# Kernel tuning notes

Measured on AMD Instinct MI355X. Metric: run time of the kernel, lower is better.

The kernel has to match this reference:

```python
import jax, jax.numpy as jnp
import numpy as np

H = 32  # hidden size

def setup_inputs() -> dict:
    key = jax.random.key(0)
    ks = jax.random.split(key, 12)
    B, T = 64, 16384
    s = 0.1
    return {
        "x": jax.random.normal(ks[0], (B, T, 1), dtype=jnp.float32),
        "h_state": jax.random.normal(ks[1], (2, B, H), dtype=jnp.float32),
        "W_ih0": jax.random.normal(ks[2], (H, 1), dtype=jnp.float32) * s,
        "W_hh0": jax.random.normal(ks[3], (H, H), dtype=jnp.float32) * s,
        "b_ih0": jax.random.normal(ks[4], (H,), dtype=jnp.float32) * s,
        "b_hh0": jax.random.normal(ks[5], (H,), dtype=jnp.float32) * s,
        "W_ih1": jax.random.normal(ks[6], (H, H), dtype=jnp.float32) * s,
        "W_hh1": jax.random.normal(ks[7], (H, H), dtype=jnp.float32) * s,
        "b_ih1": jax.random.normal(ks[8], (H,), dtype=jnp.float32) * s,
        "b_hh1": jax.random.normal(ks[9], (H,), dtype=jnp.float32) * s,
        "W_out": jax.random.normal(ks[10], (1, H), dtype=jnp.float32) * s,
        "b_out": jax.random.normal(ks[11], (1,), dtype=jnp.float32) * s,
    }

def reference(x, h_state, W_ih0, W_hh0, b_ih0, b_hh0, W_ih1, W_hh1, b_ih1, b_hh1, W_out, b_out):
    # x: [B,T,1], h_state: [2,B,H]. PyTorch RNN (tanh):
    #   h_t = tanh(W_ih x_t + b_ih + W_hh h_{t-1} + b_hh)
    # Precompute the input projection for layer 0 outside the scan (memory-bound part).
    pre0 = jnp.einsum('bti,hi->tbh', x, W_ih0) + (b_ih0 + b_hh0)  # [T,B,H]
    b1 = b_ih1 + b_hh1

    def step(carry, p0):
        h0, h1 = carry
        h0n = jnp.tanh(p0 + h0 @ W_hh0.T)
        h1n = jnp.tanh(h0n @ W_ih1.T + b1 + h1 @ W_hh1.T)
        return (h0n, h1n), h1n

    (hf0, hf1), ys = jax.lax.scan(step, (h_state[0], h_state[1]), pre0)
    r_out = jnp.transpose(ys, (1, 0, 2)).reshape(-1, H)  # [B*T, H] (batch_first view)
    outs = r_out @ W_out.T + b_out                        # [B*T, 1]
    h_final = jnp.stack([hf0, hf1])                       # [2,B,H]
    return outs, h_final
```

## Files before the change

### kernel.cpp

```cpp
#include <hip/hip_runtime.h>


#define T_LEN 16384
#define B_SZ  64
#define NW    (T_LEN / 32)
#define TSC   2.885390082f

#if __has_builtin(__builtin_amdgcn_exp2f)
#define EXP2(x) __builtin_amdgcn_exp2f(x)
#else
#define EXP2(x) exp2f(x)
#endif

typedef _Float16 h2 __attribute__((ext_vector_type(2)));

__device__ __forceinline__ float rl(float v, int lane) {
  return __int_as_float(__builtin_amdgcn_readlane(__float_as_int(v), lane));
}

__device__ __forceinline__ h2 bperm_h2(int byteaddr, h2 v) {
  int o = __builtin_amdgcn_ds_bpermute(byteaddr, __builtin_bit_cast(int, v));
  return __builtin_bit_cast(h2, o);
}

__device__ __forceinline__ float pair_swap(float v) {
  int t = __builtin_amdgcn_update_dpp(0, __float_as_int(v), 0xB1, 0xF, 0xF, true);
  return __int_as_float(t);
}

__device__ __forceinline__ float tanh_pre(float v) {
  float e = EXP2(v);
  return fmaf(-2.f, __builtin_amdgcn_rcpf(e + 1.f), 1.f);
}

#if __has_builtin(__builtin_amdgcn_fdot2)
#define FDOT2(a, b, c) __builtin_amdgcn_fdot2((a), (b), (c), false)
#else
#define FDOT2(a, b, c) \
  fmaf((float)(a).x, (float)(b).x, fmaf((float)(a).y, (float)(b).y, (c)))
#endif

__device__ __forceinline__ h2 pack_state(float hcur) {
  float hsw = pair_swap(hcur);
#if __has_builtin(__builtin_amdgcn_cvt_pkrtz)
  return __builtin_bit_cast(h2, __builtin_amdgcn_cvt_pkrtz(hcur, hsw));
#else
  h2 p; p.x = (_Float16)hcur; p.y = (_Float16)hsw; return p;
#endif
}

#define BCASTB(dst, src_pk)                                  \
  _Pragma("unroll")                                          \
  for (int j_ = 0; j_ < 16; ++j_) (dst)[j_] = bperm_h2(8 * j_, (src_pk));

__device__ __forceinline__ float dot32h(const h2* w, const h2* hb, float seed) {
  float a0 = seed, a1 = 0.f, a2 = 0.f, a3 = 0.f;
#pragma unroll
  for (int j = 0; j < 4; ++j) {
    a0 = FDOT2(w[4 * j + 0], hb[4 * j + 0], a0);
    a1 = FDOT2(w[4 * j + 1], hb[4 * j + 1], a1);
    a2 = FDOT2(w[4 * j + 2], hb[4 * j + 2], a2);
    a3 = FDOT2(w[4 * j + 3], hb[4 * j + 3], a3);
  }
  return (a0 + a1) + (a2 + a3);
}

__global__ __launch_bounds__(128, 1) void rnn2_kernel(
    const float* __restrict__ x,    const float* __restrict__ hs,
    const float* __restrict__ Wih0, const float* __restrict__ Whh0,
    const float* __restrict__ bih0, const float* __restrict__ bhh0,
    const float* __restrict__ Wih1, const float* __restrict__ Whh1,
    const float* __restrict__ bih1, const float* __restrict__ bhh1,
    const float* __restrict__ Wout, const float* __restrict__ bout,
    float* __restrict__ out)
{
  __shared__ __align__(16) float uwin[2][1024];
  __shared__ __align__(16) float scratch[1024];

  const int  tid = (int)threadIdx.x;
  const int  wv  = tid >> 6;
  const int  m   = tid & 63;
  const int  r   = m & 31;
  const bool hi  = (m >= 32);
  const int  b   = (int)blockIdx.x;

  const float* pw = (wv == 0) ? (hi ? (Wih1 + r * 32) : (Whh0 + r * 32))
                              : (hi ? Wout : (Whh1 + r * 32));
  const float wsc = (wv == 0) ? TSC : (hi ? 1.f : TSC);
  h2 w[16];
#pragma unroll
  for (int k = 0; k < 8; ++k) {
    float4 q = ((const float4*)pw)[k];
    w[2 * k].x     = (_Float16)(q.x * wsc);
    w[2 * k].y     = (_Float16)(q.y * wsc);
    w[2 * k + 1].x = (_Float16)(q.z * wsc);
    w[2 * k + 1].y = (_Float16)(q.w * wsc);
  }

  float xw = 0.f, binv = 0.f;
  if (wv == 0) {
    if (hi) binv = TSC * (bih1[r] + bhh1[r]);
    else  { binv = TSC * (bih0[r] + bhh0[r]); xw = TSC * Wih0[r]; }
  }
  const float bo = bout[0];

  float hcur = (wv == 0) ? hs[b * 32 + r] : hs[2048 + b * 32 + r];

  float* up0 = hi ? &uwin[0][r] : &scratch[r];
  float* up1 = hi ? &uwin[1][r] : &scratch[r];

  const float* xb   = x + (size_t)b * T_LEN;
  float*       outp = out + (size_t)b * T_LEN;
  float*       hf   = out + (size_t)B_SZ * T_LEN;

  float obuf = 0.f;
  float xcur = 0.f;
  if (wv == 0) xcur = xb[m];

  for (int wdx = 0; wdx <= NW; ++wdx) {
    if (wv == 0) {
      if (wdx < NW) {
        float xnext = 0.f;
        if (wdx + 1 < NW) {
          int xi = 32 * (wdx + 1) + m; if (xi > T_LEN - 1) xi = T_LEN - 1;
          xnext = xb[xi];
        }
        float* up = (wdx & 1) ? up1 : up0;
#pragma unroll 8
        for (int t2 = 0; t2 < 32; ++t2) {
          h2 hpk = pack_state(hcur);
          h2 hb[16];
          BCASTB(hb, hpk);
          float xv   = rl(xcur, t2);
          float seed = fmaf(xv, xw, binv);
          float acc  = dot32h(w, hb, seed);
          up[t2 * 32] = acc;
          hcur = tanh_pre(acc);
        }
        xcur = xnext;
      }
    } else {
      if (wdx >= 1) {
        const int wb = wdx - 1;
        const float* ub = &uwin[wb & 1][r];
        float uval = ub[0];
#pragma unroll 8
        for (int t2 = 0; t2 < 32; ++t2) {
          const int t = 32 * wb - 1 + t2;
          h2 hpk = pack_state(hcur);
          h2 hb[16];
          BCASTB(hb, hpk);
          float sB  = hi ? 0.f : uval;
          float acc = dot32h(w, hb, sB);
          float unext = ub[((t2 + 1) & 31) * 32];
          float h1n = tanh_pre(acc);
          obuf = (m == 32 + t2) ? acc : obuf;
          if (t >= 0) hcur = h1n;
          uval = unext;
        }
        const int idx = 32 * wb - 2 + r;
        if (hi && idx >= 0) outp[idx] = obuf + bo;
      }
    }
    __syncthreads();
  }

  if (wv == 0) {
    h2 hpk = pack_state(hcur);
    h2 hb[16];
    BCASTB(hb, hpk);
    float acc = dot32h(w, hb, binv);
    if (hi) uwin[0][r] = acc;
    else    hf[b * 32 + r] = hcur;
  }
  __syncthreads();

  if (wv == 1) {
    float uT = uwin[0][r];
    h2 hpk = pack_state(hcur);
    h2 hb[16];
    BCASTB(hb, hpk);
    float acc = dot32h(w, hb, hi ? 0.f : uT);
    if (m == 32) outp[T_LEN - 2] = acc + bo;
    float h1T = tanh_pre(acc);
    h2 hpk2 = pack_state(h1T);
    h2 hb2[16];
    BCASTB(hb2, hpk2);
    float acc2 = dot32h(w, hb2, 0.f);
    if (m == 32) outp[T_LEN - 1] = acc2 + bo;
    if (!hi) hf[2048 + b * 32 + r] = h1T;
  }
}

extern "C" void kernel_launch(void* const* d_in, const int* in_sizes, int n_in,
                              void* d_out, int out_size, void* d_ws, size_t ws_size,
                              hipStream_t stream) {
  rnn2_kernel<<<dim3(B_SZ), dim3(128), 0, stream>>>(
      (const float*)d_in[0],  (const float*)d_in[1],  (const float*)d_in[2],
      (const float*)d_in[3],  (const float*)d_in[4],  (const float*)d_in[5],
      (const float*)d_in[6],  (const float*)d_in[7],  (const float*)d_in[8],
      (const float*)d_in[9],  (const float*)d_in[10], (const float*)d_in[11],
      (float*)d_out);
}
```

Before: 1.838 ms.

## Split each hidden unit's dot product across lane pairs to halve broadcasts

Each wave now assigns a pair of lanes to each hidden unit, with each lane covering half of the 32-wide input. Each lane computes both the recurrent and the second matrix dot product over its 16 inputs, and the pair combines results with a DPP add. This halves the ds_bpermute broadcasts and FDOT2 chains on the serial per-timestep critical path. In exchange it adds two cross-lane reductions per step and more arithmetic per lane.

```diff
diff --git a/kernel.cpp b/kernel.cpp
--- a/kernel.cpp
+++ b/kernel.cpp
@@ -23,8 +23,13 @@
   return __builtin_bit_cast(h2, o);
 }
 
-__device__ __forceinline__ float pair_swap(float v) {
+__device__ __forceinline__ float pair_add(float v) {
   int t = __builtin_amdgcn_update_dpp(0, __float_as_int(v), 0xB1, 0xF, 0xF, true);
+  return v + __int_as_float(t);
+}
+
+__device__ __forceinline__ float quad2_swap(float v) {
+  int t = __builtin_amdgcn_update_dpp(0, __float_as_int(v), 0x4E, 0xF, 0xF, true);
   return __int_as_float(t);
 }
 
@@ -40,8 +45,8 @@
   fmaf((float)(a).x, (float)(b).x, fmaf((float)(a).y, (float)(b).y, (c)))
 #endif
 
-__device__ __forceinline__ h2 pack_state(float hcur) {
-  float hsw = pair_swap(hcur);
+__device__ __forceinline__ h2 pack_pair(float hcur) {
+  float hsw = quad2_swap(hcur);
 #if __has_builtin(__builtin_amdgcn_cvt_pkrtz)
   return __builtin_bit_cast(h2, __builtin_amdgcn_cvt_pkrtz(hcur, hsw));
 #else
@@ -49,14 +54,10 @@
 #endif
 }
 
-#define BCASTB(dst, src_pk)                                  \
-  _Pragma("unroll")                                          \
-  for (int j_ = 0; j_ < 16; ++j_) (dst)[j_] = bperm_h2(8 * j_, (src_pk));
-
-__device__ __forceinline__ float dot32h(const h2* w, const h2* hb, float seed) {
+__device__ __forceinline__ float dot16h(const h2* w, const h2* hb, float seed) {
   float a0 = seed, a1 = 0.f, a2 = 0.f, a3 = 0.f;
 #pragma unroll
-  for (int j = 0; j < 4; ++j) {
+  for (int j = 0; j < 2; ++j) {
     a0 = FDOT2(w[4 * j + 0], hb[4 * j + 0], a0);
     a1 = FDOT2(w[4 * j + 1], hb[4 * j + 1], a1);
     a2 = FDOT2(w[4 * j + 2], hb[4 * j + 2], a2);
@@ -64,6 +65,11 @@
   }
   return (a0 + a1) + (a2 + a3);
 }
+
+#define BCAST8(hb, hpk)                                        \
+  _Pragma("unroll")                                            \
+  for (int j_ = 0; j_ < 8; ++j_)                               \
+    (hb)[j_] = bperm_h2(abase + 16 * j_, (hpk));
 
 __global__ __launch_bounds__(128, 1) void rnn2_kernel(
     const float* __restrict__ x,    const float* __restrict__ hs,
@@ -80,34 +86,43 @@
   const int  tid = (int)threadIdx.x;
   const int  wv  = tid >> 6;
   const int  m   = tid & 63;
-  const int  r   = m & 31;
-  const bool hi  = (m >= 32);
+  const int  r   = m >> 1;
+  const bool q0  = !(m & 1);
   const int  b   = (int)blockIdx.x;
 
-  const float* pw = (wv == 0) ? (hi ? (Wih1 + r * 32) : (Whh0 + r * 32))
-                              : (hi ? Wout : (Whh1 + r * 32));
-  const float wsc = (wv == 0) ? TSC : (hi ? 1.f : TSC);
-  h2 w[16];
+  const int  qo  = (m & 1) * 16;
+  const float* pw1 = (wv == 0) ? (Whh0 + r * 32 + qo) : (Whh1 + r * 32 + qo);
+  const float* pw2 = (wv == 0) ? (Wih1 + r * 32 + qo) : (Wout + qo);
+  const float s2 = (wv == 0) ? TSC : 1.f;
+  h2 w1[8], w2[8];
 #pragma unroll
-  for (int k = 0; k < 8; ++k) {
-    float4 q = ((const float4*)pw)[k];
-    w[2 * k].x     = (_Float16)(q.x * wsc);
-    w[2 * k].y     = (_Float16)(q.y * wsc);
-    w[2 * k + 1].x = (_Float16)(q.z * wsc);
-    w[2 * k + 1].y = (_Float16)(q.w * wsc);
-  }
-
-  float xw = 0.f, binv = 0.f;
-  if (wv == 0) {
-    if (hi) binv = TSC * (bih1[r] + bhh1[r]);
-    else  { binv = TSC * (bih0[r] + bhh0[r]); xw = TSC * Wih0[r]; }
+  for (int k = 0; k < 4; ++k) {
+    float4 qa = ((const float4*)pw1)[k];
+    w1[2 * k].x     = (_Float16)(qa.x * TSC);
+    w1[2 * k].y     = (_Float16)(qa.y * TSC);
+    w1[2 * k + 1].x = (_Float16)(qa.z * TSC);
+    w1[2 * k + 1].y = (_Float16)(qa.w * TSC);
+    float4 qb = ((const float4*)pw2)[k];
+    w2[2 * k].x     = (_Float16)(qb.x * s2);
+    w2[2 * k].y     = (_Float16)(qb.y * s2);
+    w2[2 * k + 1].x = (_Float16)(qb.z * s2);
+    w2[2 * k + 1].y = (_Float16)(qb.w * s2);
+  }
+
+  float xw = 0.f, b1c = 0.f, b2c = 0.f;
+  if (wv == 0 && q0) {
+    xw  = TSC * Wih0[r];
+    b1c = TSC * (bih0[r] + bhh0[r]);
+    b2c = TSC * (bih1[r] + bhh1[r]);
   }
   const float bo = bout[0];
 
   float hcur = (wv == 0) ? hs[b * 32 + r] : hs[2048 + b * 32 + r];
 
-  float* up0 = hi ? &uwin[0][r] : &scratch[r];
-  float* up1 = hi ? &uwin[1][r] : &scratch[r];
+  const int abase = 128 * (m & 1);
+
+  float* up0 = q0 ? &uwin[0][r] : &scratch[m];
+  float* up1 = q0 ? &uwin[1][r] : &scratch[m];
 
   const float* xb   = x + (size_t)b * T_LEN;
   float*       outp = out + (size_t)b * T_LEN;
@@ -128,14 +143,17 @@
         float* up = (wdx & 1) ? up1 : up0;
 #pragma unroll 8
         for (int t2 = 0; t2 < 32; ++t2) {
-          h2 hpk = pack_state(hcur);
-          h2 hb[16];
-          BCASTB(hb, hpk);
-          float xv   = rl(xcur, t2);
-          float seed = fmaf(xv, xw, binv);
-          float acc  = dot32h(w, hb, seed);
-          up[t2 * 32] = acc;
-          hcur = tanh_pre(acc);
+          h2 hpk = pack_pair(hcur);
+          h2 hb[8];
+          BCAST8(hb, hpk);
+          float xv    = rl(xcur, t2);
+          float seed1 = fmaf(xv, xw, b1c);
+          float acc1 = dot16h(w1, hb, seed1);
+          float acc2 = dot16h(w2, hb, b2c);
+          float a1f = pair_add(acc1);
+          float a2f = pair_add(acc2);
+          up[t2 * 32] = a2f;
+          hcur = tanh_pre(a1f);
         }
         xcur = xnext;
       }
@@ -147,48 +165,55 @@
 #pragma unroll 8
         for (int t2 = 0; t2 < 32; ++t2) {
           const int t = 32 * wb - 1 + t2;
-          h2 hpk = pack_state(hcur);
-          h2 hb[16];
-          BCASTB(hb, hpk);
-          float sB  = hi ? 0.f : uval;
-          float acc = dot32h(w, hb, sB);
+          h2 hpk = pack_pair(hcur);
+          h2 hb[8];
+          BCAST8(hb, hpk);
+          float seed1 = q0 ? uval : 0.f;
+          float acc1 = dot16h(w1, hb, seed1);
+          float acc2 = dot16h(w2, hb, 0.f);
           float unext = ub[((t2 + 1) & 31) * 32];
-          float h1n = tanh_pre(acc);
-          obuf = (m == 32 + t2) ? acc : obuf;
+          float a1f = pair_add(acc1);
+          float a2f = pair_add(acc2);
+          float h1n = tanh_pre(a1f);
+          obuf = (m == t2) ? a2f : obuf;
           if (t >= 0) hcur = h1n;
           uval = unext;
         }
-        const int idx = 32 * wb - 2 + r;
-        if (hi && idx >= 0) outp[idx] = obuf + bo;
+        const int idx = 32 * wb - 2 + m;
+        if (m < 32 && idx >= 0) outp[idx] = obuf + bo;
       }
     }
     __syncthreads();
   }
 
   if (wv == 0) {
-    h2 hpk = pack_state(hcur);
-    h2 hb[16];
-    BCASTB(hb, hpk);
-    float acc = dot32h(w, hb, binv);
-    if (hi) uwin[0][r] = acc;
-    else    hf[b * 32 + r] = hcur;
+    h2 hpk = pack_pair(hcur);
+    h2 hb[8];
+    BCAST8(hb, hpk);
+    float acc2 = dot16h(w2, hb, b2c);
+    float a2f = pair_add(acc2);
+    if (q0) { uwin[0][r] = a2f; hf[b * 32 + r] = hcur; }
   }
   __syncthreads();
 
   if (wv == 1) {
     float uT = uwin[0][r];
-    h2 hpk = pack_state(hcur);
-    h2 hb[16];
-    BCASTB(hb, hpk);
-    float acc = dot32h(w, hb, hi ? 0.f : uT);
-    if (m == 32) outp[T_LEN - 2] = acc + bo;
-    float h1T = tanh_pre(acc);
-    h2 hpk2 = pack_state(h1T);
-    h2 hb2[16];
-    BCASTB(hb2, hpk2);
-    float acc2 = dot32h(w, hb2, 0.f);
-    if (m == 32) outp[T_LEN - 1] = acc2 + bo;
-    if (!hi) hf[2048 + b * 32 + r] = h1T;
+    h2 hpk = pack_pair(hcur);
+    h2 hb[8];
+    BCAST8(hb, hpk);
+    float acc1 = dot16h(w1, hb, q0 ? uT : 0.f);
+    float acc2 = dot16h(w2, hb, 0.f);
+    float a1f = pair_add(acc1);
+    float a2f = pair_add(acc2);
+    if (m == 0) outp[T_LEN - 2] = a2f + bo;
+    float h1T = tanh_pre(a1f);
+    h2 hpk2 = pack_pair(h1T);
+    h2 hb2[8];
+    BCAST8(hb2, hpk2);
+    float acc2b = dot16h(w2, hb2, 0.f);
+    float a2bf = pair_add(acc2b);
+    if (m == 0) outp[T_LEN - 1] = a2bf + bo;
+    if (q0) hf[2048 + b * 32 + r] = h1T;
   }
 }
 
```

Measured after the change: 2.529 ms. 1.38x slower.
